# Kernel tuning notes

Measured on AMD Instinct MI355X. Metric: run time of the kernel, lower is better.

The kernel has to match this reference:

```python
import jax, jax.numpy as jnp
import numpy as np

# MLA dims (DeepSeek-V2-Lite-class)
B, S, D = 2, 2048, 2048
H = 16
NOPE, ROPE, VD = 128, 64, 128   # qk_nope_head_dim, qk_rope_head_dim, v_head_dim
KV_RANK, Q_RANK = 512, 1536
EPS = 1e-6
THETA = 10000.0


def setup_inputs() -> dict:
    key = jax.random.key(0)
    ks = jax.random.split(key, 8)

    def init(k, shape, fan_in):
        return jax.random.normal(k, shape, jnp.float32) * (fan_in ** -0.5)

    return {
        "x": jax.random.normal(ks[0], (B, S, D), jnp.float32),
        "w_dq": init(ks[1], (D, Q_RANK), D),
        "q_a_norm": jnp.ones((Q_RANK,), jnp.float32),
        "w_uq": init(ks[2], (Q_RANK, H * (NOPE + ROPE)), Q_RANK),
        "w_dkv": init(ks[3], (D, KV_RANK + ROPE), D),
        "kv_a_norm": jnp.ones((KV_RANK,), jnp.float32),
        "w_ukv": init(ks[4], (KV_RANK, H * (NOPE + VD)), KV_RANK),
        "w_o": init(ks[5], (H * VD, D), H * VD),
    }


def _rmsnorm(x, w):
    return x * jax.lax.rsqrt(jnp.mean(x * x, axis=-1, keepdims=True) + EPS) * w


def _rope(x):
    # x: [B, S, H', d] -> rotary on last dim (half-split style)
    d = x.shape[-1]
    inv = 1.0 / (THETA ** (jnp.arange(0, d, 2, dtype=jnp.float32) / d))
    ang = jnp.arange(x.shape[1], dtype=jnp.float32)[:, None] * inv[None, :]  # [S, d/2]
    cos = jnp.cos(ang)[None, :, None, :]
    sin = jnp.sin(ang)[None, :, None, :]
    x1, x2 = jnp.split(x, 2, axis=-1)
    return jnp.concatenate([x1 * cos - x2 * sin, x2 * cos + x1 * sin], axis=-1)


def reference(x, w_dq, q_a_norm, w_uq, w_dkv, kv_a_norm, w_ukv, w_o):
    # --- low-rank Q projection ---
    q = _rmsnorm(x @ w_dq, q_a_norm) @ w_uq          # [B,S,H*(NOPE+ROPE)]
    q = q.reshape(B, S, H, NOPE + ROPE)
    q_nope, q_pe = q[..., :NOPE], q[..., NOPE:]

    # --- latent (compressed) KV projection + shared decoupled-RoPE key ---
    ckv = x @ w_dkv                                   # [B,S,KV_RANK+ROPE]
    c_kv, k_pe = ckv[..., :KV_RANK], ckv[..., KV_RANK:]
    kv = (_rmsnorm(c_kv, kv_a_norm) @ w_ukv).reshape(B, S, H, NOPE + VD)
    k_nope, v = kv[..., :NOPE], kv[..., NOPE:]

    # --- decoupled RoPE on rope dims only ---
    q_pe = _rope(q_pe)                                # [B,S,H,ROPE]
    k_pe = _rope(k_pe[:, :, None, :])                 # [B,S,1,ROPE] shared across heads

    qf = jnp.concatenate([q_nope, q_pe], axis=-1)     # [B,S,H,NOPE+ROPE]
    kf = jnp.concatenate([k_nope, jnp.broadcast_to(k_pe, (B, S, H, ROPE))], axis=-1)

    # --- scaled dot-product attention with causal mask ---
    scale = 1.0 / jnp.sqrt(jnp.float32(NOPE + ROPE))
    scores = jnp.einsum("bqhd,bkhd->bhqk", qf * scale, kf)  # [B,H,S,S]
    causal = jnp.tril(jnp.ones((S, S), bool))
    scores = jnp.where(causal[None, None], scores, -1e9)
    w = jax.nn.softmax(scores, axis=-1)
    o = jnp.einsum("bhqk,bkhd->bqhd", w, v).reshape(B, S, H * VD)
    return o @ w_o                                    # [B,S,D]
```

## Files before the change

kernel.cpp:

```cpp
#include <hip/hip_runtime.h>
#include <hip/hip_bf16.h>
#include <math.h>

#define SS 2048
#define HH 16
#define EPSF 1e-6f
#define MR 4096
#define L2T 13.287712379549449f
#define ASCL (0.07216878364870322f * 1.4426950408889634f)

typedef unsigned short u16;
typedef unsigned int u32;
typedef __attribute__((ext_vector_type(8))) short bf8_t;
typedef __attribute__((ext_vector_type(4))) float f4_t;

__device__ inline u16 f2b(float f) {
    __hip_bfloat16 h = __float2bfloat16(f);
    return __builtin_bit_cast(u16, h);
}
__device__ inline float b2f(u16 x) {
    u32 v = (u32)x << 16;
    return __builtin_bit_cast(float, v);
}

#define GLD16(g, l) __builtin_amdgcn_global_load_lds( \
    (const __attribute__((address_space(1))) u32*)(g), \
    (__attribute__((address_space(3))) u32*)(l), 16, 0, 0)

#define MFMA16(a,b,c) __builtin_amdgcn_mfma_f32_16x16x32_bf16((a),(b),(c),0,0,0)

__global__ void prep_k(const float* __restrict__ x, u16* __restrict__ xb,
                       const float* __restrict__ w_dq, const float* __restrict__ w_dkv,
                       const float* __restrict__ w_uq, const float* __restrict__ w_ukv,
                       const float* __restrict__ w_o,
                       u16* __restrict__ wT1, u16* __restrict__ wTuq,
                       u16* __restrict__ wTukv, u16* __restrict__ wTo) {
    __shared__ float tt[32][33];
    int blk = blockIdx.x, tid = threadIdx.x;
    if (blk < 8192) {
        int i = blk * 256 + tid;
        float4 v = ((const float4*)x)[i];
        ushort4 o;
        o.x = f2b(v.x); o.y = f2b(v.y); o.z = f2b(v.z); o.w = f2b(v.w);
        *(ushort4*)(xb + (size_t)i * 4) = o;
        return;
    }
    blk -= 8192;
    const float* W; u16* dst; int K, N, Npad, nx;
    if (blk < 3072)       { W = w_dq;  dst = wT1;                      K = 2048; N = 1536; Npad = 1536; nx = 48; }
    else if (blk < 4352)  { blk -= 3072; W = w_dkv; dst = wT1 + (size_t)1536 * 2048; K = 2048; N = 576;  Npad = 640;  nx = 20; }
    else if (blk < 8960)  { blk -= 4352; W = w_uq;  dst = wTuq;        K = 1536; N = 3072; Npad = 3072; nx = 96; }
    else if (blk < 11008) { blk -= 8960; W = w_ukv; dst = wTukv;       K = 512;  N = 4096; Npad = 4096; nx = 128; }
    else                  { blk -= 11008; W = w_o;  dst = wTo;         K = 2048; N = 2048; Npad = 2048; nx = 64; }
    int n0 = (blk % nx) * 32, k0 = (blk / nx) * 32;
    int tx = tid & 31, ty = tid >> 5;
    for (int i = ty; i < 32; i += 8) {
        int n = n0 + tx;
        tt[i][tx] = (n < N) ? W[(size_t)(k0 + i) * N + n] : 0.f;
    }
    __syncthreads();
    for (int i = ty; i < 32; i += 8) {
        int n = n0 + i;
        if (n < Npad) dst[(size_t)n * K + k0 + tx] = f2b(tt[tx][i]);
    }
}

template <int MODE, int MINW>
__global__ __launch_bounds__(256, MINW)
void gemm_mfma(const u16* __restrict__ A, const u16* __restrict__ BT,
               void* __restrict__ Cv, void* __restrict__ Cv2, int K, int N) {
    __shared__ u16 lA[128 * 32];
    __shared__ u16 lB[128 * 32];
    const int tid = threadIdx.x;
    const int w = tid >> 6, lane = tid & 63;
    const int quad = lane >> 4, col = lane & 15;
    const int wm = (w >> 1) * 64, wn = (w & 1) * 64;
    const int bm = blockIdx.y * 128, bn = blockIdx.x * 128;
    const int srow = lane >> 2;
    const int scol = (lane & 3) * 8;
    f4_t acc[4][4] = {};
    for (int k0 = 0; k0 < K; k0 += 32) {
        __syncthreads();
        #pragma unroll
        for (int cc = 0; cc < 2; cc++) {
            int c = 2 * w + cc;
            int row = c * 16 + srow;
            GLD16(A  + (size_t)(bm + row) * K + k0 + scol, (char*)lA + c * 1024);
            GLD16(BT + (size_t)(bn + row) * K + k0 + scol, (char*)lB + c * 1024);
        }
        __syncthreads();
        bf8_t af[4], bf[4];
        #pragma unroll
        for (int i = 0; i < 4; i++) {
            af[i] = *(const bf8_t*)(lA + (wm + i * 16 + col) * 32 + quad * 8);
            bf[i] = *(const bf8_t*)(lB + (wn + i * 16 + col) * 32 + quad * 8);
        }
        #pragma unroll
        for (int mi = 0; mi < 4; mi++)
            #pragma unroll
            for (int ni = 0; ni < 4; ni++)
                acc[mi][ni] = MFMA16(af[mi], bf[ni], acc[mi][ni]);
    }
    if (MODE == 0) {
        float* C = (float*)Cv;
        #pragma unroll
        for (int mi = 0; mi < 4; mi++)
            #pragma unroll
            for (int ni = 0; ni < 4; ni++) {
                int n = bn + wn + ni * 16 + col;
                #pragma unroll
                for (int r = 0; r < 4; r++) {
                    int m = bm + wm + mi * 16 + quad * 4 + r;
                    C[(size_t)m * N + n] = acc[mi][ni][r];
                }
            }
    } else if (MODE == 1) {
        u16* C = (u16*)Cv;
        #pragma unroll
        for (int mi = 0; mi < 4; mi++)
            #pragma unroll
            for (int ni = 0; ni < 4; ni++) {
                int n = bn + wn + ni * 16 + col;
                #pragma unroll
                for (int r = 0; r < 4; r++) {
                    int m = bm + wm + mi * 16 + quad * 4 + r;
                    C[(size_t)m * N + n] = f2b(acc[mi][ni][r]);
                }
            }
    } else if (MODE == 2) {
        u16* C = (u16*)Cv;
        int span = ((bn + wn) >> 6) % 3;
        if (span < 2) {
            #pragma unroll
            for (int mi = 0; mi < 4; mi++)
                #pragma unroll
                for (int ni = 0; ni < 4; ni++) {
                    int n = bn + wn + ni * 16 + col;
                    #pragma unroll
                    for (int r = 0; r < 4; r++) {
                        int m = bm + wm + mi * 16 + quad * 4 + r;
                        C[(size_t)m * N + n] = f2b(acc[mi][ni][r] * ASCL);
                    }
                }
        } else {
            #pragma unroll
            for (int ni = 0; ni < 2; ni++) {
                int e = ni * 16 + col;
                float inv = exp2f(-(float)e * (L2T / 32.0f));
                #pragma unroll
                for (int mi = 0; mi < 4; mi++) {
                    #pragma unroll
                    for (int r = 0; r < 4; r++) {
                        int m = bm + wm + mi * 16 + quad * 4 + r;
                        int pos = m & (SS - 1);
                        float ang = (float)pos * inv;
                        float cs, sn; sincosf(ang, &sn, &cs);
                        float x1 = acc[mi][ni][r], x2 = acc[mi][ni + 2][r];
                        int n = bn + wn + ni * 16 + col;
                        C[(size_t)m * N + n]      = f2b((x1 * cs - x2 * sn) * ASCL);
                        C[(size_t)m * N + n + 32] = f2b((x2 * cs + x1 * sn) * ASCL);
                    }
                }
            }
        }
    } else {
        u16* kb = (u16*)Cv;
        u16* vT = (u16*)Cv2;
        #pragma unroll
        for (int ni = 0; ni < 4; ni++) {
            int nb = bn + wn + ni * 16;
            int h = nb >> 8;
            int cb = nb & 255;
            if (cb < 128) {
                #pragma unroll
                for (int mi = 0; mi < 4; mi++)
                    #pragma unroll
                    for (int r = 0; r < 4; r++) {
                        int m = bm + wm + mi * 16 + quad * 4 + r;
                        kb[((size_t)m * HH + h) * 192 + cb + col] = f2b(acc[mi][ni][r]);
                    }
            } else {
                int dv = cb - 128 + col;
                #pragma unroll
                for (int mi = 0; mi < 4; mi++) {
                    int mb = bm + wm + mi * 16 + quad * 4;
                    ushort4 o;
                    o.x = f2b(acc[mi][ni][0]);
                    o.y = f2b(acc[mi][ni][1]);
                    o.z = f2b(acc[mi][ni][2]);
                    o.w = f2b(acc[mi][ni][3]);
                    *(ushort4*)(vT + ((size_t)h * 128 + dv) * 4096 + mb) = o;
                }
            }
        }
    }
}

__global__ void rms_all_k(const u16* __restrict__ C1, const float* __restrict__ wq,
                          const float* __restrict__ wkv,
                          u16* __restrict__ qlb, u16* __restrict__ ckvnb,
                          u16* __restrict__ kb) {
    __shared__ float red[256];
    int tid = threadIdx.x;
    if (blockIdx.x < 4096) {
        int row = blockIdx.x;
        const ushort4* rp = (const ushort4*)(C1 + (size_t)row * 2176);
        float s = 0.f;
        for (int i = tid; i < 384; i += 256) {
            ushort4 u = rp[i];
            float a = b2f(u.x), b = b2f(u.y), c = b2f(u.z), d = b2f(u.w);
            s += a * a + b * b + c * c + d * d;
        }
        red[tid] = s;
        __syncthreads();
        for (int off = 128; off > 0; off >>= 1) {
            if (tid < off) red[tid] += red[tid + off];
            __syncthreads();
        }
        float sc = rsqrtf(red[0] * (1.0f / 1536.0f) + EPSF);
        ushort4* op = (ushort4*)(qlb + (size_t)row * 1536);
        const float4* wv = (const float4*)wq;
        for (int i = tid; i < 384; i += 256) {
            ushort4 u = rp[i];
            float4 ww = wv[i];
            ushort4 o;
            o.x = f2b(b2f(u.x) * sc * ww.x);
            o.y = f2b(b2f(u.y) * sc * ww.y);
            o.z = f2b(b2f(u.z) * sc * ww.z);
            o.w = f2b(b2f(u.w) * sc * ww.w);
            op[i] = o;
        }
    } else {
        int row = blockIdx.x - 4096;
        const u16* base = C1 + (size_t)row * 2176 + 1536;
        if (tid < 32) {
            int t = tid;
            float x1 = b2f(base[512 + t]), x2 = b2f(base[544 + t]);
            int pos = row & (SS - 1);
            float inv = exp2f(-(float)t * (L2T / 32.0f));
            float ang = (float)pos * inv;
            float cs, sn; sincosf(ang, &sn, &cs);
            u16 y1 = f2b(x1 * cs - x2 * sn);
            u16 y2 = f2b(x2 * cs + x1 * sn);
            u16* kr = kb + (size_t)row * HH * 192;
            #pragma unroll
            for (int h = 0; h < HH; h++) {
                kr[h * 192 + 128 + t] = y1;
                kr[h * 192 + 160 + t] = y2;
            }
        }
        const ushort4* rp = (const ushort4*)base;
        float s = 0.f;
        if (tid < 128) {
            ushort4 u = rp[tid];
            float a = b2f(u.x), b = b2f(u.y), c = b2f(u.z), d = b2f(u.w);
            s = a * a + b * b + c * c + d * d;
        }
        red[tid] = s;
        __syncthreads();
        for (int off = 128; off > 0; off >>= 1) {
            if (tid < off) red[tid] += red[tid + off];
            __syncthreads();
        }
        float sc = rsqrtf(red[0] * (1.0f / 512.0f) + EPSF);
        if (tid < 128) {
            ushort4 u = rp[tid];
            float4 ww = ((const float4*)wkv)[tid];
            ushort4 o;
            o.x = f2b(b2f(u.x) * sc * ww.x);
            o.y = f2b(b2f(u.y) * sc * ww.y);
            o.z = f2b(b2f(u.z) * sc * ww.z);
            o.w = f2b(b2f(u.w) * sc * ww.w);
            ((ushort4*)(ckvnb + (size_t)row * 512))[tid] = o;
        }
    }
}

__global__ __launch_bounds__(256, 3)
void attn_mfma(const u16* __restrict__ qb, const u16* __restrict__ kb,
               const u16* __restrict__ vT, u16* __restrict__ ob) {
    __shared__ u16 lK[64 * 200];
    __shared__ u16 lV[128 * 72];
    __shared__ u16 lP[4 * 16 * 72];
    const int tid = threadIdx.x, w = tid >> 6, lane = tid & 63;
    const int quad = lane >> 4, col = lane & 15;
    const int bh = blockIdx.x, b = bh >> 4, h = bh & 15;
    const int qt = 31 - (int)blockIdx.y;
    const int tok0 = b * SS;
    int goff[11];
    #pragma unroll
    for (int jj = 0; jj < 11; jj++) {
        int c = w + 4 * jj;
        if (c < 25) {
            int o = c * 1024 + lane * 16;
            int row = o / 400, ro = o - row * 400;
            goff[jj] = (ro < 384) ? (row * HH + h) * 192 + (ro >> 1) : 0;
        } else {
            int c2 = c - 25;
            int o = c2 * 1024 + lane * 16;
            int row = o / 144, ro = o - row * 144;
            goff[jj] = (ro < 128) ? (h * 128 + row) * 4096 + (ro >> 1) : 0;
        }
    }
    u16* pw = lP + w * 16 * 72;
    bf8_t qf[6];
    {
        int qtok = tok0 + qt * 64 + w * 16 + col;
        const u16* qp = qb + ((size_t)qtok * HH + h) * 192 + quad * 8;
        #pragma unroll
        for (int kc = 0; kc < 6; kc++) qf[kc] = *(const bf8_t*)(qp + kc * 32);
    }
    f4_t o[8] = {};
    float mrow[4] = {-1e30f, -1e30f, -1e30f, -1e30f};
    float lrow[4] = {0.f, 0.f, 0.f, 0.f};
    for (int kt = 0; kt <= qt; kt++) {
        size_t kbase = (size_t)(tok0 + kt * 64) * (HH * 192);
        size_t vbase = (size_t)(tok0 + kt * 64);
        __syncthreads();
        #pragma unroll
        for (int jj = 0; jj < 11; jj++) {
            int c = w + 4 * jj;
            if (c < 25)      GLD16(kb + kbase + goff[jj], (char*)lK + c * 1024);
            else if (c < 43) GLD16(vT + vbase + goff[jj], (char*)lV + (c - 25) * 1024);
        }
        __syncthreads();
        bool diag = (kt == qt);
        f4_t s[4] = {};
        #pragma unroll
        for (int t = 0; t < 4; t++) {
            if (!diag || t <= w) {
                #pragma unroll
                for (int kc = 0; kc < 6; kc++) {
                    bf8_t kf = *(const bf8_t*)(lK + (t * 16 + col) * 200 + kc * 32 + quad * 8);
                    s[t] = MFMA16(qf[kc], kf, s[t]);
                }
            }
        }
        if (diag) {
            #pragma unroll
            for (int t = 0; t < 4; t++) {
                int kg = t * 16 + col;
                #pragma unroll
                for (int r = 0; r < 4; r++) {
                    int qg = w * 16 + quad * 4 + r;
                    if (kg > qg) s[t][r] = -1e30f;
                }
            }
        }
        float sm[4] = {-1e30f, -1e30f, -1e30f, -1e30f};
        #pragma unroll
        for (int t = 0; t < 4; t++)
            #pragma unroll
            for (int r = 0; r < 4; r++) sm[r] = fmaxf(sm[r], s[t][r]);
        #pragma unroll
        for (int off = 1; off < 16; off <<= 1)
            #pragma unroll
            for (int r = 0; r < 4; r++) sm[r] = fmaxf(sm[r], __shfl_xor(sm[r], off));
        float al[4];
        #pragma unroll
        for (int r = 0; r < 4; r++) {
            float mn = fmaxf(mrow[r], sm[r]);
            al[r] = exp2f(mrow[r] - mn);
            mrow[r] = mn;
        }
        float rs[4] = {0.f, 0.f, 0.f, 0.f};
        #pragma unroll
        for (int t = 0; t < 4; t++)
            #pragma unroll
            for (int r = 0; r < 4; r++) {
                float p = exp2f(s[t][r] - mrow[r]);
                s[t][r] = p;
                rs[r] += p;
            }
        #pragma unroll
        for (int off = 1; off < 16; off <<= 1)
            #pragma unroll
            for (int r = 0; r < 4; r++) rs[r] += __shfl_xor(rs[r], off);
        #pragma unroll
        for (int r = 0; r < 4; r++) lrow[r] = lrow[r] * al[r] + rs[r];
        #pragma unroll
        for (int n = 0; n < 8; n++)
            #pragma unroll
            for (int r = 0; r < 4; r++) o[n][r] *= al[r];
        #pragma unroll
        for (int t = 0; t < 4; t++)
            #pragma unroll
            for (int r = 0; r < 4; r++)
                pw[(quad * 4 + r) * 72 + t * 16 + col] = f2b(s[t][r]);
        #pragma unroll
        for (int kc2 = 0; kc2 < 2; kc2++) {
            bf8_t pf = *(const bf8_t*)(pw + col * 72 + kc2 * 32 + quad * 8);
            #pragma unroll
            for (int n = 0; n < 8; n++) {
                bf8_t vf = *(const bf8_t*)(lV + (n * 16 + col) * 72 + kc2 * 32 + quad * 8);
                o[n] = MFMA16(pf, vf, o[n]);
            }
        }
    }
    #pragma unroll
    for (int n = 0; n < 8; n++)
        #pragma unroll
        for (int r = 0; r < 4; r++) {
            int qtok = tok0 + qt * 64 + w * 16 + quad * 4 + r;
            ob[((size_t)qtok * HH + h) * 128 + n * 16 + col] = f2b(o[n][r] / lrow[r]);
        }
}

extern "C" void kernel_launch(void* const* d_in, const int* in_sizes, int n_in,
                              void* d_out, int out_size, void* d_ws, size_t ws_size,
                              hipStream_t stream) {
    const float* x        = (const float*)d_in[0];
    const float* w_dq     = (const float*)d_in[1];
    const float* q_a_norm = (const float*)d_in[2];
    const float* w_uq     = (const float*)d_in[3];
    const float* w_dkv    = (const float*)d_in[4];
    const float* kv_a_nrm = (const float*)d_in[5];
    const float* w_ukv    = (const float*)d_in[6];
    const float* w_o      = (const float*)d_in[7];
    float* out = (float*)d_out;

    char* ws = (char*)d_ws;
    const size_t MB = 1024 * 1024;
    u16* xb    = (u16*)(ws);
    u16* wT1   = (u16*)(ws + 17 * MB);
    u16* wTuq  = (u16*)(ws + 26 * MB);
    u16* wTukv = (u16*)(ws + 36 * MB);
    u16* wTo   = (u16*)(ws + 41 * MB);
    u16* C1    = (u16*)(ws + 50 * MB);
    u16* qlb   = (u16*)(ws + 68 * MB);
    u16* qbuf  = (u16*)(ws + 81 * MB);
    u16* ckvnb = (u16*)(ws + 107 * MB);
    u16* kb    = (u16*)(ws + 112 * MB);
    u16* vT    = (u16*)(ws + 138 * MB);
    u16* aob   = xb;

    prep_k<<<23296, 256, 0, stream>>>(x, xb, w_dq, w_dkv, w_uq, w_ukv, w_o,
                                      wT1, wTuq, wTukv, wTo);
    gemm_mfma<1, 3><<<dim3(17, 32), 256, 0, stream>>>(xb, wT1, C1, nullptr, 2048, 2176);
    rms_all_k<<<8192, 256, 0, stream>>>(C1, q_a_norm, kv_a_nrm, qlb, ckvnb, kb);
    gemm_mfma<2, 2><<<dim3(24, 32), 256, 0, stream>>>(qlb, wTuq, qbuf, nullptr, 1536, 3072);
    gemm_mfma<3, 3><<<dim3(32, 32), 256, 0, stream>>>(ckvnb, wTukv, kb, vT, 512, 4096);
    attn_mfma<<<dim3(32, 32), 256, 0, stream>>>(qbuf, kb, vT, aob);
    gemm_mfma<0, 3><<<dim3(16, 32), 256, 0, stream>>>(aob, wTo, out, nullptr, 2048, 2048);
}
```

Baseline: 452.3 us.

## Double attention query tile per block and transpose V via LDS in epilogue

Each attention block now processes 128 query rows (two 16-row slices per wave), so every K/V tile loaded into LDS serves twice the queries and V fragments are read from LDS once per tile. The grid is halved, with a reordered query-tile schedule that interleaves heavy and light causal tiles, and occupancy bounds are lowered to 2. The V-transposed epilogue of the KV up-projection GEMM stages through shared memory so global writes become contiguous 16-byte stores instead of scattered 8-byte ones. The costs are extra register pressure, lower occupancy, and an added LDS buffer in the GEMM.

```diff
diff --git a/kernel.cpp b/kernel.cpp
--- a/kernel.cpp
+++ b/kernel.cpp
@@ -101,7 +101,7 @@
             for (int ni = 0; ni < 4; ni++)
                 acc[mi][ni] = MFMA16(af[mi], bf[ni], acc[mi][ni]);
     }
-    if (MODE == 0) {
+    if constexpr (MODE == 0) {
         float* C = (float*)Cv;
         #pragma unroll
         for (int mi = 0; mi < 4; mi++)
@@ -114,7 +114,7 @@
                     C[(size_t)m * N + n] = acc[mi][ni][r];
                 }
             }
-    } else if (MODE == 1) {
+    } else if constexpr (MODE == 1) {
         u16* C = (u16*)Cv;
         #pragma unroll
         for (int mi = 0; mi < 4; mi++)
@@ -127,7 +127,7 @@
                     C[(size_t)m * N + n] = f2b(acc[mi][ni][r]);
                 }
             }
-    } else if (MODE == 2) {
+    } else if constexpr (MODE == 2) {
         u16* C = (u16*)Cv;
         int span = ((bn + wn) >> 6) % 3;
         if (span < 2) {
@@ -166,12 +166,11 @@
     } else {
         u16* kb = (u16*)Cv;
         u16* vT = (u16*)Cv2;
-        #pragma unroll
-        for (int ni = 0; ni < 4; ni++) {
-            int nb = bn + wn + ni * 16;
-            int h = nb >> 8;
-            int cb = nb & 255;
-            if (cb < 128) {
+        int h = blockIdx.x >> 1;
+        if ((blockIdx.x & 1) == 0) {
+            #pragma unroll
+            for (int ni = 0; ni < 4; ni++) {
+                int cb = wn + ni * 16;
                 #pragma unroll
                 for (int mi = 0; mi < 4; mi++)
                     #pragma unroll
@@ -179,18 +178,29 @@
                         int m = bm + wm + mi * 16 + quad * 4 + r;
                         kb[((size_t)m * HH + h) * 192 + cb + col] = f2b(acc[mi][ni][r]);
                     }
-            } else {
-                int dv = cb - 128 + col;
+            }
+        } else {
+            __shared__ u16 sc[4][64][72];
+            u16 (*scw)[72] = sc[w];
+            #pragma unroll
+            for (int ni = 0; ni < 4; ni++) {
+                int dvl = ni * 16 + col;
                 #pragma unroll
                 for (int mi = 0; mi < 4; mi++) {
-                    int mb = bm + wm + mi * 16 + quad * 4;
                     ushort4 o;
                     o.x = f2b(acc[mi][ni][0]);
                     o.y = f2b(acc[mi][ni][1]);
                     o.z = f2b(acc[mi][ni][2]);
                     o.w = f2b(acc[mi][ni][3]);
-                    *(ushort4*)(vT + ((size_t)h * 128 + dv) * 4096 + mb) = o;
-                }
+                    *(ushort4*)&scw[dvl][mi * 16 + quad * 4] = o;
+                }
+            }
+            #pragma unroll
+            for (int cc = 0; cc < 8; cc++) {
+                int dvl = cc * 8 + (lane >> 3);
+                int t8 = lane & 7;
+                bf8_t vv = *(const bf8_t*)&scw[dvl][t8 * 8];
+                *(bf8_t*)(vT + ((size_t)(h * 128 + wn + dvl)) * 4096 + bm + wm + t8 * 8) = vv;
             }
         }
     }
@@ -276,7 +286,7 @@
     }
 }
 
-__global__ __launch_bounds__(256, 3)
+__global__ __launch_bounds__(256, 2)
 void attn_mfma(const u16* __restrict__ qb, const u16* __restrict__ kb,
                const u16* __restrict__ vT, u16* __restrict__ ob) {
     __shared__ u16 lK[64 * 200];
@@ -285,7 +295,8 @@
     const int tid = threadIdx.x, w = tid >> 6, lane = tid & 63;
     const int quad = lane >> 4, col = lane & 15;
     const int bh = blockIdx.x, b = bh >> 4, h = bh & 15;
-    const int qt = 31 - (int)blockIdx.y;
+    const int y = blockIdx.y;
+    const int qt = (y < 8) ? (15 - y) : (y - 8);
     const int tok0 = b * SS;
     int goff[11];
     #pragma unroll
@@ -303,19 +314,28 @@
         }
     }
     u16* pw = lP + w * 16 * 72;
-    bf8_t qf[6];
-    {
-        int qtok = tok0 + qt * 64 + w * 16 + col;
+    const int qb0 = qt * 128 + w * 32;
+    const int qb1 = qb0 + 16;
+    bf8_t qf[2][6];
+    #pragma unroll
+    for (int m = 0; m < 2; m++) {
+        int qtok = tok0 + qb0 + m * 16 + col;
         const u16* qp = qb + ((size_t)qtok * HH + h) * 192 + quad * 8;
         #pragma unroll
-        for (int kc = 0; kc < 6; kc++) qf[kc] = *(const bf8_t*)(qp + kc * 32);
-    }
-    f4_t o[8] = {};
-    float mrow[4] = {-1e30f, -1e30f, -1e30f, -1e30f};
-    float lrow[4] = {0.f, 0.f, 0.f, 0.f};
-    for (int kt = 0; kt <= qt; kt++) {
-        size_t kbase = (size_t)(tok0 + kt * 64) * (HH * 192);
-        size_t vbase = (size_t)(tok0 + kt * 64);
+        for (int kc = 0; kc < 6; kc++) qf[m][kc] = *(const bf8_t*)(qp + kc * 32);
+    }
+    f4_t o[2][8] = {};
+    float mrow[2][4], lrow[2][4];
+    #pragma unroll
+    for (int m = 0; m < 2; m++)
+        #pragma unroll
+        for (int r = 0; r < 4; r++) { mrow[m][r] = -1e30f; lrow[m][r] = 0.f; }
+
+    const int nkt = 2 * qt + 2;
+    for (int kt = 0; kt < nkt; kt++) {
+        const int kt64 = kt * 64;
+        size_t kbase = (size_t)(tok0 + kt64) * (HH * 192);
+        size_t vbase = (size_t)(tok0 + kt64);
         __syncthreads();
         #pragma unroll
         for (int jj = 0; jj < 11; jj++) {
@@ -324,86 +344,104 @@
             else if (c < 43) GLD16(vT + vbase + goff[jj], (char*)lV + (c - 25) * 1024);
         }
         __syncthreads();
-        bool diag = (kt == qt);
-        f4_t s[4] = {};
+        f4_t s[2][4] = {};
         #pragma unroll
         for (int t = 0; t < 4; t++) {
-            if (!diag || t <= w) {
+            int kb_l = kt64 + t * 16;
+            if (kb_l <= qb1) {
+                bool m0 = (kb_l <= qb0);
                 #pragma unroll
                 for (int kc = 0; kc < 6; kc++) {
                     bf8_t kf = *(const bf8_t*)(lK + (t * 16 + col) * 200 + kc * 32 + quad * 8);
-                    s[t] = MFMA16(qf[kc], kf, s[t]);
-                }
-            }
-        }
-        if (diag) {
-            #pragma unroll
-            for (int t = 0; t < 4; t++) {
-                int kg = t * 16 + col;
-                #pragma unroll
-                for (int r = 0; r < 4; r++) {
-                    int qg = w * 16 + quad * 4 + r;
-                    if (kg > qg) s[t][r] = -1e30f;
-                }
-            }
-        }
-        float sm[4] = {-1e30f, -1e30f, -1e30f, -1e30f};
-        #pragma unroll
-        for (int t = 0; t < 4; t++)
-            #pragma unroll
-            for (int r = 0; r < 4; r++) sm[r] = fmaxf(sm[r], s[t][r]);
-        #pragma unroll
-        for (int off = 1; off < 16; off <<= 1)
-            #pragma unroll
-            for (int r = 0; r < 4; r++) sm[r] = fmaxf(sm[r], __shfl_xor(sm[r], off));
-        float al[4];
-        #pragma unroll
-        for (int r = 0; r < 4; r++) {
-            float mn = fmaxf(mrow[r], sm[r]);
-            al[r] = exp2f(mrow[r] - mn);
-            mrow[r] = mn;
-        }
-        float rs[4] = {0.f, 0.f, 0.f, 0.f};
-        #pragma unroll
-        for (int t = 0; t < 4; t++)
+                    s[1][t] = MFMA16(qf[1][kc], kf, s[1][t]);
+                    if (m0) s[0][t] = MFMA16(qf[0][kc], kf, s[0][t]);
+                }
+            }
+        }
+        if (kt64 <= qb1) {
+            #pragma unroll
+            for (int m = 0; m < 2; m++) {
+                int qbm = qb0 + m * 16;
+                #pragma unroll
+                for (int t = 0; t < 4; t++) {
+                    int kb_l = kt64 + t * 16;
+                    if (kb_l >= qbm) {
+                        int kg = kb_l + col;
+                        #pragma unroll
+                        for (int r = 0; r < 4; r++)
+                            if (kg > qbm + quad * 4 + r) s[m][t][r] = -1e30f;
+                    }
+                }
+            }
+            bf8_t vf[2][8];
+            #pragma unroll
+            for (int kc2 = 0; kc2 < 2; kc2++)
+                #pragma unroll
+                for (int n = 0; n < 8; n++)
+                    vf[kc2][n] = *(const bf8_t*)(lV + (n * 16 + col) * 72 + kc2 * 32 + quad * 8);
+            #pragma unroll
+            for (int m = 0; m < 2; m++) {
+                if (kt64 <= qb0 + m * 16) {
+                    float sm[4] = {-1e30f, -1e30f, -1e30f, -1e30f};
+                    #pragma unroll
+                    for (int t = 0; t < 4; t++)
+                        #pragma unroll
+                        for (int r = 0; r < 4; r++) sm[r] = fmaxf(sm[r], s[m][t][r]);
+                    #pragma unroll
+                    for (int off = 1; off < 16; off <<= 1)
+                        #pragma unroll
+                        for (int r = 0; r < 4; r++) sm[r] = fmaxf(sm[r], __shfl_xor(sm[r], off));
+                    float al[4];
+                    #pragma unroll
+                    for (int r = 0; r < 4; r++) {
+                        float mn = fmaxf(mrow[m][r], sm[r]);
+                        al[r] = exp2f(mrow[m][r] - mn);
+                        mrow[m][r] = mn;
+                    }
+                    float rs[4] = {0.f, 0.f, 0.f, 0.f};
+                    #pragma unroll
+                    for (int t = 0; t < 4; t++)
+                        #pragma unroll
+                        for (int r = 0; r < 4; r++) {
+                            float p = exp2f(s[m][t][r] - mrow[m][r]);
+                            s[m][t][r] = p;
+                            rs[r] += p;
+                        }
+                    #pragma unroll
+                    for (int off = 1; off < 16; off <<= 1)
+                        #pragma unroll
+                        for (int r = 0; r < 4; r++) rs[r] += __shfl_xor(rs[r], off);
+                    #pragma unroll
+                    for (int r = 0; r < 4; r++) lrow[m][r] = lrow[m][r] * al[r] + rs[r];
+                    #pragma unroll
+                    for (int n = 0; n < 8; n++)
+                        #pragma unroll
+                        for (int r = 0; r < 4; r++) o[m][n][r] *= al[r];
+                    #pragma unroll
+                    for (int t = 0; t < 4; t++)
+                        #pragma unroll
+                        for (int r = 0; r < 4; r++)
+                            pw[(quad * 4 + r) * 72 + t * 16 + col] = f2b(s[m][t][r]);
+                    #pragma unroll
+                    for (int kc2 = 0; kc2 < 2; kc2++) {
+                        bf8_t pf = *(const bf8_t*)(pw + col * 72 + kc2 * 32 + quad * 8);
+                        #pragma unroll
+                        for (int n = 0; n < 8; n++)
+                            o[m][n] = MFMA16(pf, vf[kc2][n], o[m][n]);
+                    }
+                }
+            }
+        }
+    }
+    #pragma unroll
+    for (int m = 0; m < 2; m++)
+        #pragma unroll
+        for (int n = 0; n < 8; n++)
             #pragma unroll
             for (int r = 0; r < 4; r++) {
-                float p = exp2f(s[t][r] - mrow[r]);
-                s[t][r] = p;
-                rs[r] += p;
-            }
-        #pragma unroll
-        for (int off = 1; off < 16; off <<= 1)
-            #pragma unroll
-            for (int r = 0; r < 4; r++) rs[r] += __shfl_xor(rs[r], off);
-        #pragma unroll
-        for (int r = 0; r < 4; r++) lrow[r] = lrow[r] * al[r] + rs[r];
-        #pragma unroll
-        for (int n = 0; n < 8; n++)
-            #pragma unroll
-            for (int r = 0; r < 4; r++) o[n][r] *= al[r];
-        #pragma unroll
-        for (int t = 0; t < 4; t++)
-            #pragma unroll
-            for (int r = 0; r < 4; r++)
-                pw[(quad * 4 + r) * 72 + t * 16 + col] = f2b(s[t][r]);
-        #pragma unroll
-        for (int kc2 = 0; kc2 < 2; kc2++) {
-            bf8_t pf = *(const bf8_t*)(pw + col * 72 + kc2 * 32 + quad * 8);
-            #pragma unroll
-            for (int n = 0; n < 8; n++) {
-                bf8_t vf = *(const bf8_t*)(lV + (n * 16 + col) * 72 + kc2 * 32 + quad * 8);
-                o[n] = MFMA16(pf, vf, o[n]);
-            }
-        }
-    }
-    #pragma unroll
-    for (int n = 0; n < 8; n++)
-        #pragma unroll
-        for (int r = 0; r < 4; r++) {
-            int qtok = tok0 + qt * 64 + w * 16 + quad * 4 + r;
-            ob[((size_t)qtok * HH + h) * 128 + n * 16 + col] = f2b(o[n][r] / lrow[r]);
-        }
+                int qtok = tok0 + qb0 + m * 16 + quad * 4 + r;
+                ob[((size_t)qtok * HH + h) * 128 + n * 16 + col] = f2b(o[m][n][r] / lrow[m][r]);
+            }
 }
 
 extern "C" void kernel_launch(void* const* d_in, const int* in_sizes, int n_in,
@@ -439,7 +477,7 @@
     gemm_mfma<1, 3><<<dim3(17, 32), 256, 0, stream>>>(xb, wT1, C1, nullptr, 2048, 2176);
     rms_all_k<<<8192, 256, 0, stream>>>(C1, q_a_norm, kv_a_nrm, qlb, ckvnb, kb);
     gemm_mfma<2, 2><<<dim3(24, 32), 256, 0, stream>>>(qlb, wTuq, qbuf, nullptr, 1536, 3072);
-    gemm_mfma<3, 3><<<dim3(32, 32), 256, 0, stream>>>(ckvnb, wTukv, kb, vT, 512, 4096);
-    attn_mfma<<<dim3(32, 32), 256, 0, stream>>>(qbuf, kb, vT, aob);
+    gemm_mfma<3, 2><<<dim3(32, 32), 256, 0, stream>>>(ckvnb, wTukv, kb, vT, 512, 4096);
+    attn_mfma<<<dim3(32, 16), 256, 0, stream>>>(qbuf, kb, vT, aob);
     gemm_mfma<0, 3><<<dim3(16, 32), 256, 0, stream>>>(aob, wTo, out, nullptr, 2048, 2048);
 }
```

New measurement: 594.7 us. +31.5%, slower.
